# Performance work log

Measured on AMD Instinct MI355X. Metric: run time of the kernel, lower is better.

The kernel has to match this reference:

```python
import jax, jax.numpy as jnp
import numpy as np

D_MODEL = 1024
N_HEADS = 16
D_K = 64  # per-head dim and the scaling denominator used by the module
NEG = -1e9  # stand-in for -inf in masked_fill (rows are never fully masked)


def setup_inputs() -> dict:
    key = jax.random.key(0)
    ks = jax.random.split(key, 8)
    B, M, N = 2, 2048, 2048
    q = jax.random.normal(ks[0], (B, M, D_MODEL), dtype=jnp.float32)
    k = jax.random.normal(ks[1], (B, N, D_MODEL), dtype=jnp.float32)
    v = jax.random.normal(ks[2], (B, N, D_MODEL), dtype=jnp.float32)
    mask = jax.random.randint(ks[3], (B, M, N), 0, 2).astype(jnp.bool_)
    # xavier_uniform for square [d,d] weights: limit = sqrt(6/(d+d))
    lim = float(np.sqrt(6.0 / (D_MODEL + D_MODEL)))
    Wq = jax.random.uniform(ks[4], (D_MODEL, D_MODEL), jnp.float32, -lim, lim)
    Wk = jax.random.uniform(ks[5], (D_MODEL, D_MODEL), jnp.float32, -lim, lim)
    Wv = jax.random.uniform(ks[6], (D_MODEL, D_MODEL), jnp.float32, -lim, lim)
    Wo = jax.random.uniform(ks[7], (D_MODEL, D_MODEL), jnp.float32, -lim, lim)
    return {"q": q, "k": k, "v": v, "mask": mask,
            "Wq": Wq, "Wk": Wk, "Wv": Wv, "Wo": Wo}


def _split_heads(x):
    # (B, S, D) -> (B, H, S, Dh); the torch split/cat-on-batch trick is
    # mathematically identical to this standard head reshape.
    B, S, _ = x.shape
    return x.reshape(B, S, N_HEADS, D_K).transpose(0, 2, 1, 3)


def reference(q, k, v, mask, Wq, Wk, Wv, Wo):
    qw = _split_heads(q @ Wq.T)  # (B,H,M,Dh)
    kw = _split_heads(k @ Wk.T)  # (B,H,N,Dh)
    vw = _split_heads(v @ Wv.T)  # (B,H,N,Dh)
    scores = jnp.einsum('bhmd,bhnd->bhmn', qw, kw)
    scores = jnp.where(mask[:, None, :, :], NEG, scores)
    attn = jax.nn.softmax(scores / jnp.sqrt(jnp.float32(D_K)), axis=-1)
    ctx = jnp.einsum('bhmn,bhnd->bhmd', attn, vw)
    B, _, M, _ = ctx.shape
    ctx = ctx.transpose(0, 2, 1, 3).reshape(B, M, D_MODEL)
    return ctx @ Wo.T
```

## Files before the change

kernel.cpp:

```cpp
#include <hip/hip_runtime.h>
#include <hip/hip_bf16.h>
#include <stdint.h>
#include <string.h>

#define SEQ   2048
#define DM    1024
#define NH    16
#define NB    2

typedef __attribute__((ext_vector_type(8))) short bf16x8;
typedef __attribute__((ext_vector_type(4))) float f32x4;
typedef unsigned short u16;
typedef unsigned int   u32;

__device__ __forceinline__ u16 f2bf(float f) {
    u32 u = __float_as_uint(f);
    u += 0x7FFF + ((u >> 16) & 1);
    return (u16)(u >> 16);
}
__device__ __forceinline__ u32 pk2bf(float a, float b) {
    __hip_bfloat162 p = __float22bfloat162_rn(make_float2(a, b));
    u32 u; memcpy(&u, &p, 4); return u;
}
__device__ __forceinline__ float fexp2(float x) {
#if __has_builtin(__builtin_amdgcn_exp2f)
    return __builtin_amdgcn_exp2f(x);
#else
    return exp2f(x);
#endif
}
__device__ __forceinline__ float mask_exp2(float s, u32 lsel, int pos) {
#if __has_builtin(__builtin_amdgcn_sbfe)
    u32 keep = (u32)__builtin_amdgcn_sbfe((int)lsel, pos, 1);
#else
    u32 keep = (u32)((int)(lsel << (31 - pos)) >> 31);
#endif
    return __uint_as_float(__float_as_uint(fexp2(s)) & keep);
}
__device__ __forceinline__ void gl_lds16(const void* g, void* l) {
    __builtin_amdgcn_global_load_lds(
        (const __attribute__((address_space(1))) u32*)g,
        (__attribute__((address_space(3))) u32*)l, 16, 0, 0);
}
__device__ __forceinline__ void wbar_vm3() { asm volatile("s_waitcnt vmcnt(3)\ns_barrier" ::: "memory"); }
__device__ __forceinline__ void wbar_vm4() { asm volatile("s_waitcnt vmcnt(4)\ns_barrier" ::: "memory"); }
__device__ __forceinline__ void vm_drain() { asm volatile("s_waitcnt vmcnt(0)" ::: "memory"); }

struct CvtArgs {
    const float* s[7];
    u16* d[7];
    float scale[7];
    int start[8];
    const int* mask;
    u32* mbits;
};
__global__ __launch_bounds__(256) void cvt_kernel(CvtArgs a) {
    int bid = blockIdx.x;
    int tid = threadIdx.x;
    if (bid >= 8192) {
        int widx = (bid - 8192) * 256 + tid;
        uint4 v = ((const uint4*)a.mask)[widx];
        unsigned long long b0 = __ballot(v.x != 0);
        unsigned long long b1 = __ballot(v.y != 0);
        unsigned long long b2 = __ballot(v.z != 0);
        unsigned long long b3 = __ballot(v.w != 0);
        int lane = tid & 63;
        if (lane < 4) {
            int sh = lane * 16;
            u32 lo = (u32)((b0 >> sh) & 0xFFFF) | ((u32)((b1 >> sh) & 0xFFFF) << 16);
            u32 hi = (u32)((b2 >> sh) & 0xFFFF) | ((u32)((b3 >> sh) & 0xFFFF) << 16);
            size_t N = (size_t)(bid - 8192) * 1024 + (size_t)(tid >> 6) * 256
                     + (size_t)lane * 64;
            u32* dst = a.mbits + ((N >> 11) * 64 + ((N >> 6) & 31) * 2);
            *(uint2*)dst = make_uint2(lo, hi);
        }
        return;
    }
    int seg = 0;
#pragma unroll
    for (int i = 1; i < 7; ++i) if (bid >= a.start[i]) seg = i;
    float sc = a.scale[seg];
    size_t base = (size_t)(bid - a.start[seg]) * 2048 + tid * 8;
    const float4* s4 = (const float4*)(a.s[seg] + base);
    float4 x = s4[0], y = s4[1];
    u32 r[4];
    r[0] = pk2bf(x.x*sc, x.y*sc); r[1] = pk2bf(x.z*sc, x.w*sc);
    r[2] = pk2bf(y.x*sc, y.y*sc); r[3] = pk2bf(y.z*sc, y.w*sc);
    *(uint4*)(a.d[seg] + base) = *(uint4*)r;
}

template<int RT>
__device__ __forceinline__ void gemm_body(const u16* __restrict__ A,
                                          const u16* __restrict__ Bm,
                                          void* __restrict__ Y,
                                          int rtile, int ctile, int mode,
                                          u16* sA, u16* sB) {
    constexpr int ABUF = RT * 32 * 32;
    constexpr int BBUF = 128 * 32;
    const int tid  = threadIdx.x;
    const int wv   = tid >> 6, lane = tid & 63;
    const int quad = lane >> 4, ln = lane & 15;
    const int wr   = wv >> 1,  wc  = wv & 1;

    const int lr4 = lane >> 2;
    const int lcc = ((lane & 3) ^ ((lane >> 3) & 3)) * 8;

    const u16* gA[RT/2]; u16* lA[RT/2];
#pragma unroll
    for (int s = 0; s < RT/2; ++s) {
        int seg = wv * (RT/2) + s;
        gA[s] = A + (size_t)(rtile * (RT*32) + seg*16 + lr4) * 1024 + lcc;
        lA[s] = sA + seg * 512;
    }
    const u16* gB[2]; u16* lB[2];
#pragma unroll
    for (int s = 0; s < 2; ++s) {
        int seg = wv * 2 + s;
        gB[s] = Bm + (size_t)(ctile * 128 + seg*16 + lr4) * 1024 + lcc;
        lB[s] = sB + seg * 512;
    }

    f32x4 acc[RT][4];
#pragma unroll
    for (int i = 0; i < RT; ++i)
#pragma unroll
        for (int j = 0; j < 4; ++j) acc[i][j] = (f32x4){0.f,0.f,0.f,0.f};

    const int c0 = (quad ^ ((ln >> 1) & 3)) * 8;

#pragma unroll
    for (int s = 0; s < RT/2; ++s) gl_lds16(gA[s], lA[s]);
#pragma unroll
    for (int s = 0; s < 2; ++s)    gl_lds16(gB[s], lB[s]);
#pragma unroll
    for (int s = 0; s < RT/2; ++s) gl_lds16(gA[s] + 32, lA[s] + ABUF);
#pragma unroll
    for (int s = 0; s < 2; ++s)    gl_lds16(gB[s] + 32, lB[s] + BBUF);

    int bc = 0, bp = 2;
    for (int kt = 0; kt < 32; ++kt) {
        if (RT == 4) wbar_vm4(); else wbar_vm3();
        int pk = (kt + 2) & 31;
#pragma unroll
        for (int s = 0; s < RT/2; ++s) gl_lds16(gA[s] + pk*32, lA[s] + bp*ABUF);
#pragma unroll
        for (int s = 0; s < 2; ++s)    gl_lds16(gB[s] + pk*32, lB[s] + bp*BBUF);

        const u16* sAb = sA + bc * ABUF;
        const u16* sBb = sB + bc * BBUF;
        bf16x8 af[RT], bfr[4];
#pragma unroll
        for (int rt = 0; rt < RT; ++rt)
            af[rt] = *(const bf16x8*)(sAb + (wr*(RT*16) + rt*16 + ln) * 32 + c0);
#pragma unroll
        for (int ct = 0; ct < 4; ++ct)
            bfr[ct] = *(const bf16x8*)(sBb + (wc*64 + ct*16 + ln) * 32 + c0);
#pragma unroll
        for (int rt = 0; rt < RT; ++rt)
#pragma unroll
            for (int ct = 0; ct < 4; ++ct)
                acc[rt][ct] = __builtin_amdgcn_mfma_f32_16x16x32_bf16(
                    af[rt], bfr[ct], acc[rt][ct], 0, 0, 0);

        bc = (bc == 2) ? 0 : bc + 1;
        bp = (bp == 2) ? 0 : bp + 1;
    }
    vm_drain();

#pragma unroll
    for (int rt = 0; rt < RT; ++rt) {
#pragma unroll
        for (int ct = 0; ct < 4; ++ct) {
#pragma unroll
            for (int i = 0; i < 4; ++i) {
                int R = rtile*(RT*32) + wr*(RT*16) + rt*16 + quad*4 + i;
                int C = ctile*128 + wc*64 + ct*16 + ln;
                float val = acc[rt][ct][i];
                if (mode == 0) {
                    int b = R >> 11, s = R & 2047, h = C >> 6, d = C & 63;
                    ((u16*)Y)[((size_t)((b*NH + h) * SEQ + s) << 6) + d] = f2bf(val);
                } else if (mode == 1) {
                    int h = R >> 6, d = R & 63, b = C >> 11, n = C & 2047;
                    int nl = n & 63;
                    int np = (nl & 32) | (((nl & 15) >> 2) << 3) | (nl & 3)
                           | ((nl & 16) >> 2);
                    n = (n & ~63) | np;
                    ((u16*)Y)[((size_t)((b*NH + h) * 64 + d) << 11) + n] = f2bf(val);
                } else {
                    ((float*)Y)[(size_t)R * 1024 + C] = val;
                }
            }
        }
    }
}

struct QKVArgs { const u16* A[3]; const u16* B[3]; u16* Y[3]; };

__global__ __launch_bounds__(256) void gemm_qkv(QKVArgs g) {
    __shared__ u16 sA[3 * 128 * 32];
    __shared__ u16 sB[3 * 128 * 32];
    int z = blockIdx.z;
    if (z == 2)
        gemm_body<4>(g.A[2], g.B[2], g.Y[2], blockIdx.y, blockIdx.x, 1, sA, sB);
    else
        gemm_body<4>(g.A[z], g.B[z], g.Y[z], blockIdx.x, blockIdx.y, 0, sA, sB);
}

__global__ __launch_bounds__(256) void gemm_out(const u16* __restrict__ A,
                                                const u16* __restrict__ Bm,
                                                float* __restrict__ Y) {
    __shared__ u16 sA[3 * 64 * 32];
    __shared__ u16 sB[3 * 128 * 32];
    gemm_body<2>(A, Bm, Y, blockIdx.x, blockIdx.y, 2, sA, sB);
}

__global__ __launch_bounds__(512, 4) void attn_kernel(
    const u16* __restrict__ qw,
    const u16* __restrict__ kw,
    const u16* __restrict__ vt,
    const u32* __restrict__ mbits,
    u16* __restrict__ ctx) {

    __shared__ __align__(16) u16 smem[32768];
    u16* sK = smem;
    u16* sV = smem + 16384;

    const int mtile = blockIdx.x;
    const int bh    = blockIdx.y;
    const int b     = bh >> 4;
    const int tid   = threadIdx.x;
    const int wv    = tid >> 6, lane = tid & 63;
    const int quad  = lane >> 4, ln = lane & 15;
    const int m0    = mtile * 128;

    const size_t hbase = (size_t)bh * SEQ * 64;

    bf16x8 qf[2];
    {
        const u16* qp = qw + hbase + (size_t)(m0 + wv*16 + ln) * 64 + quad*8;
        qf[0] = *(const bf16x8*)(qp);
        qf[1] = *(const bf16x8*)(qp + 32);
    }

    f32x4 o[4], lsum;
    lsum = (f32x4){0.f,0.f,0.f,0.f};
#pragma unroll
    for (int j = 0; j < 4; ++j) o[j] = (f32x4){0.f,0.f,0.f,0.f};

    bf16x8 ones;
#pragma unroll
    for (int i = 0; i < 8; ++i) ones[i] = (short)0x3F80;

    const u32* mrow = mbits + (size_t)(b*SEQ + m0 + wv*16 + ln) * 64;

    const int lr = lane >> 3;
    const int lc = (lane & 7) ^ lr;
    const u16* gK = kw + hbase + (size_t)(wv*8 + lr) * 64 + lc*8;
    const u16* gV = vt + hbase + (size_t)(wv*8 + lr) * SEQ + lc*8;
    u16* lK = sK + wv * 512;
    u16* lV = sV + wv * 512;

    const int c0 = (quad ^ (ln & 7)) * 8;
    const u16* a1 = smem + ln*64 + c0;
    const u16* a2 = smem + ln*64 + (c0 ^ 32);

    gl_lds16(gK, lK);
    gl_lds16(gV, lV);
    uint2 wwA = *(const uint2*)(mrow);
    gl_lds16(gK + 4096, lK + 4096);
    gl_lds16(gV + 64,   lV + 4096);
    uint2 wwB = *(const uint2*)(mrow + 2);

    for (int mi = 0; mi < 8; ++mi) {
#pragma unroll
        for (int u = 0; u < 4; ++u) {
            const int bc = u;
            const int wb = (u + 2) & 3;
            wbar_vm3();
            int pidx = (mi*4 + u + 2) & 31;
            gl_lds16(gK + (size_t)pidx * 4096, lK + wb*4096);
            gl_lds16(gV + pidx * 64,           lV + wb*4096);
            uint2 wwC = *(const uint2*)(mrow + pidx*2);

            f32x4 s4[4];
            __builtin_amdgcn_s_setprio(1);
#pragma unroll
            for (int ct = 0; ct < 4; ++ct) {
                bf16x8 k0 = *(const bf16x8*)(a1 + bc*4096 + ct*1024);
                bf16x8 k1 = *(const bf16x8*)(a2 + bc*4096 + ct*1024);
                f32x4 z = (f32x4){0.f, 0.f, 0.f, 0.f};
                z = __builtin_amdgcn_mfma_f32_16x16x32_bf16(k0, qf[0], z, 0, 0, 0);
                z = __builtin_amdgcn_mfma_f32_16x16x32_bf16(k1, qf[1], z, 0, 0, 0);
                s4[ct] = z;
            }
            __builtin_amdgcn_s_setprio(0);

            u32 P0[4], P1[4];
            {
                u32 l0 = ~(wwA.x >> quad);
                u32 l1 = ~(wwA.y >> quad);
#pragma unroll
                for (int ct = 0; ct < 4; ++ct) {
                    float p[4];
                    p[0] = mask_exp2(s4[ct][0], l0, ct*4);
                    p[1] = mask_exp2(s4[ct][1], l0, 16 + ct*4);
                    p[2] = mask_exp2(s4[ct][2], l1, ct*4);
                    p[3] = mask_exp2(s4[ct][3], l1, 16 + ct*4);
                    u32 lo = pk2bf(p[0], p[1]);
                    u32 hi = pk2bf(p[2], p[3]);
                    if (ct == 0)      { P0[0] = lo; P0[1] = hi; }
                    else if (ct == 1) { P0[2] = lo; P0[3] = hi; }
                    else if (ct == 2) { P1[0] = lo; P1[1] = hi; }
                    else              { P1[2] = lo; P1[3] = hi; }
                }
            }
            bf16x8 pf0, pf1;
            memcpy(&pf0, P0, 16);
            memcpy(&pf1, P1, 16);

            __builtin_amdgcn_s_setprio(1);
            lsum = __builtin_amdgcn_mfma_f32_16x16x32_bf16(pf0, ones, lsum, 0, 0, 0);
            lsum = __builtin_amdgcn_mfma_f32_16x16x32_bf16(pf1, ones, lsum, 0, 0, 0);
#pragma unroll
            for (int ct = 0; ct < 4; ++ct) {
                bf16x8 vf0 = *(const bf16x8*)(a1 + 16384 + bc*4096 + ct*1024);
                bf16x8 vf1 = *(const bf16x8*)(a2 + 16384 + bc*4096 + ct*1024);
                o[ct] = __builtin_amdgcn_mfma_f32_16x16x32_bf16(pf0, vf0, o[ct], 0, 0, 0);
                o[ct] = __builtin_amdgcn_mfma_f32_16x16x32_bf16(pf1, vf1, o[ct], 0, 0, 0);
            }
            __builtin_amdgcn_s_setprio(0);

            wwA = wwB; wwB = wwC;
        }
    }
    vm_drain();

#pragma unroll
    for (int i = 0; i < 4; ++i) {
        float inv = 1.f / lsum[i];
        int m = m0 + wv*16 + quad*4 + i;
        size_t base = ((size_t)(b * SEQ + m) << 10) + (bh & 15) * 64;
#pragma unroll
        for (int ct = 0; ct < 4; ++ct)
            ctx[base + ct*16 + ln] = f2bf(o[ct][i] * inv);
    }
}

extern "C" void kernel_launch(void* const* d_in, const int* in_sizes, int n_in,
                              void* d_out, int out_size, void* d_ws, size_t ws_size,
                              hipStream_t stream) {
    const float* q    = (const float*)d_in[0];
    const float* k    = (const float*)d_in[1];
    const float* v    = (const float*)d_in[2];
    const int*   mask = (const int*)d_in[3];
    const float* Wq   = (const float*)d_in[4];
    const float* Wk   = (const float*)d_in[5];
    const float* Wv   = (const float*)d_in[6];
    const float* Wo   = (const float*)d_in[7];
    float* out = (float*)d_out;

    char* ws = (char*)d_ws;
    const size_t SZH = (size_t)NB * SEQ * DM * 2;
    const size_t SZW = (size_t)DM * DM * 2;
    u16* qw   = (u16*)(ws);
    u16* kw   = (u16*)(ws + SZH);
    u16* vt   = (u16*)(ws + 2*SZH);
    u16* ctx  = (u16*)(ws + 3*SZH);
    u16* vb   = ctx;
    u32* mbits= (u32*)(ws + 4*SZH);
    u16* qb   = (u16*)(ws + 4*SZH + (1u<<20));
    u16* kb   = (u16*)(ws + 4*SZH + (1u<<20) + SZH);
    u16* Wqb  = (u16*)(ws + 4*SZH + (1u<<20) + 2*SZH);
    u16* Wkb  = (u16*)((char*)Wqb + SZW);
    u16* Wvb  = (u16*)((char*)Wqb + 2*SZW);
    u16* Wob  = (u16*)((char*)Wqb + 3*SZW);

    const float CSC = 0.18033688011112042f;

    CvtArgs ca;
    ca.s[0]=q;  ca.d[0]=qb;  ca.scale[0]=1.f;
    ca.s[1]=k;  ca.d[1]=kb;  ca.scale[1]=1.f;
    ca.s[2]=v;  ca.d[2]=vb;  ca.scale[2]=1.f;
    ca.s[3]=Wq; ca.d[3]=Wqb; ca.scale[3]=CSC;
    ca.s[4]=Wk; ca.d[4]=Wkb; ca.scale[4]=1.f;
    ca.s[5]=Wv; ca.d[5]=Wvb; ca.scale[5]=1.f;
    ca.s[6]=Wo; ca.d[6]=Wob; ca.scale[6]=1.f;
    int st[8] = {0, 2048, 4096, 6144, 6656, 7168, 7680, 8192};
    for (int i = 0; i < 8; ++i) ca.start[i] = st[i];
    ca.mask  = mask;
    ca.mbits = mbits;
    cvt_kernel<<<dim3(16384), dim3(256), 0, stream>>>(ca);

    QKVArgs ga;
    ga.A[0]=qb;  ga.B[0]=Wqb; ga.Y[0]=qw;
    ga.A[1]=kb;  ga.B[1]=Wkb; ga.Y[1]=kw;
    ga.A[2]=Wvb; ga.B[2]=vb;  ga.Y[2]=vt;
    gemm_qkv<<<dim3(32, 8, 3), dim3(256), 0, stream>>>(ga);

    attn_kernel<<<dim3(SEQ/128, NB*NH), dim3(512), 0, stream>>>(qw, kw, vt, mbits, ctx);

    gemm_out<<<dim3(64, 8), dim3(256), 0, stream>>>(ctx, Wob, out);
}
```

Measured before the change: 242.8 us.

## Fuse conversion and QKV projection into one cooperative kernel with grid sync

Merges the fp32-to-bf16 conversion/mask-bitpacking kernel and the QKV projection GEMM into one cooperative kernel of 768 persistent blocks. The conversion work is grid-strided, then a grid-wide sync separates it from the GEMM tiles, which are remapped so neighbouring blocks share tiles. This removes one kernel launch and its ramp-down/ramp-up gap. It adds a grid barrier cost and lowers parallelism in the conversion phase, and it falls back to the two separate launches if the cooperative launch fails.

Result: slower. 358.4 us (+47.6%).

```diff
diff --git a/kernel.cpp b/kernel.cpp
--- a/kernel.cpp
+++ b/kernel.cpp
@@ -1,7 +1,10 @@
 #include <hip/hip_runtime.h>
 #include <hip/hip_bf16.h>
+#include <hip/hip_cooperative_groups.h>
 #include <stdint.h>
 #include <string.h>
+
+namespace cg = cooperative_groups;
 
 #define SEQ   2048
 #define DM    1024
@@ -54,11 +57,10 @@
     const int* mask;
     u32* mbits;
 };
-__global__ __launch_bounds__(256) void cvt_kernel(CvtArgs a) {
-    int bid = blockIdx.x;
+__device__ __forceinline__ void cvt_work(const CvtArgs& a, int vb) {
     int tid = threadIdx.x;
-    if (bid >= 8192) {
-        int widx = (bid - 8192) * 256 + tid;
+    if (vb >= 8192) {
+        int widx = (vb - 8192) * 256 + tid;
         uint4 v = ((const uint4*)a.mask)[widx];
         unsigned long long b0 = __ballot(v.x != 0);
         unsigned long long b1 = __ballot(v.y != 0);
@@ -69,7 +71,7 @@
             int sh = lane * 16;
             u32 lo = (u32)((b0 >> sh) & 0xFFFF) | ((u32)((b1 >> sh) & 0xFFFF) << 16);
             u32 hi = (u32)((b2 >> sh) & 0xFFFF) | ((u32)((b3 >> sh) & 0xFFFF) << 16);
-            size_t N = (size_t)(bid - 8192) * 1024 + (size_t)(tid >> 6) * 256
+            size_t N = (size_t)(vb - 8192) * 1024 + (size_t)(tid >> 6) * 256
                      + (size_t)lane * 64;
             u32* dst = a.mbits + ((N >> 11) * 64 + ((N >> 6) & 31) * 2);
             *(uint2*)dst = make_uint2(lo, hi);
@@ -78,15 +80,19 @@
     }
     int seg = 0;
 #pragma unroll
-    for (int i = 1; i < 7; ++i) if (bid >= a.start[i]) seg = i;
+    for (int i = 1; i < 7; ++i) if (vb >= a.start[i]) seg = i;
     float sc = a.scale[seg];
-    size_t base = (size_t)(bid - a.start[seg]) * 2048 + tid * 8;
+    size_t base = (size_t)(vb - a.start[seg]) * 2048 + tid * 8;
     const float4* s4 = (const float4*)(a.s[seg] + base);
     float4 x = s4[0], y = s4[1];
     u32 r[4];
     r[0] = pk2bf(x.x*sc, x.y*sc); r[1] = pk2bf(x.z*sc, x.w*sc);
     r[2] = pk2bf(y.x*sc, y.y*sc); r[3] = pk2bf(y.z*sc, y.w*sc);
     *(uint4*)(a.d[seg] + base) = *(uint4*)r;
+}
+
+__global__ __launch_bounds__(256) void cvt_kernel(CvtArgs a) {
+    cvt_work(a, blockIdx.x);
 }
 
 template<int RT>
@@ -206,6 +212,23 @@
         gemm_body<4>(g.A[z], g.B[z], g.Y[z], blockIdx.x, blockIdx.y, 0, sA, sB);
 }
 
+__global__ __launch_bounds__(256, 3) void fused_pre(CvtArgs ca, QKVArgs ga) {
+    for (int it = 0; it < 22; ++it) {
+        int vb = it * 768 + (int)blockIdx.x;
+        if (vb < 16384) cvt_work(ca, vb);
+    }
+    cg::this_grid().sync();
+    __shared__ u16 sA[3 * 128 * 32];
+    __shared__ u16 sB[3 * 128 * 32];
+    int x = (int)blockIdx.x & 7, j = (int)blockIdx.x >> 3;
+    int t = x * 96 + j;
+    int z = t >> 8, rem = t & 255;
+    if (z == 2)
+        gemm_body<4>(ga.A[2], ga.B[2], ga.Y[2], rem & 7, rem >> 3, 1, sA, sB);
+    else
+        gemm_body<4>(ga.A[z], ga.B[z], ga.Y[z], rem >> 3, rem & 7, 0, sA, sB);
+}
+
 __global__ __launch_bounds__(256) void gemm_out(const u16* __restrict__ A,
                                                 const u16* __restrict__ Bm,
                                                 float* __restrict__ Y) {
@@ -389,13 +412,21 @@
     for (int i = 0; i < 8; ++i) ca.start[i] = st[i];
     ca.mask  = mask;
     ca.mbits = mbits;
-    cvt_kernel<<<dim3(16384), dim3(256), 0, stream>>>(ca);
 
     QKVArgs ga;
     ga.A[0]=qb;  ga.B[0]=Wqb; ga.Y[0]=qw;
     ga.A[1]=kb;  ga.B[1]=Wkb; ga.Y[1]=kw;
     ga.A[2]=Wvb; ga.B[2]=vb;  ga.Y[2]=vt;
-    gemm_qkv<<<dim3(32, 8, 3), dim3(256), 0, stream>>>(ga);
+
+    void* kargs[] = { (void*)&ca, (void*)&ga };
+    hipError_t ce = hipLaunchCooperativeKernel((const void*)fused_pre,
+                                               dim3(768), dim3(256),
+                                               kargs, 0, stream);
+    if (ce != hipSuccess) {
+        (void)hipGetLastError();
+        cvt_kernel<<<dim3(16384), dim3(256), 0, stream>>>(ca);
+        gemm_qkv<<<dim3(32, 8, 3), dim3(256), 0, stream>>>(ga);
+    }
 
     attn_kernel<<<dim3(SEQ/128, NB*NH), dim3(512), 0, stream>>>(qw, kw, vt, mbits, ctx);
 
```

## Split key columns across two wave groups so each K/V fragment serves two query tiles

Applied to the files above, without the earlier changes.

The attention kernel's eight waves are regrouped into two groups of four. Each wave now owns 32 query rows (two 16-row tiles) and handles half of each key block, so every K and V fragment read from LDS feeds two MFMA tiles instead of one. The two groups' partial outputs and row sums are combined through LDS at the end before normalisation and the bf16 store. This cuts LDS read traffic per MFMA. In exchange it adds register pressure, an extra mask-word load per step, and a shared-memory reduction with two extra barriers in the epilogue.

Result: slower. 251.2 us, median of 2 (+3.5%).

```diff
diff --git a/kernel.cpp b/kernel.cpp
--- a/kernel.cpp
+++ b/kernel.cpp
@@ -231,27 +231,34 @@
     const int tid   = threadIdx.x;
     const int wv    = tid >> 6, lane = tid & 63;
     const int quad  = lane >> 4, ln = lane & 15;
+    const int g     = wv >> 2;
+    const int w2    = wv & 3;
     const int m0    = mtile * 128;
 
     const size_t hbase = (size_t)bh * SEQ * 64;
 
-    bf16x8 qf[2];
-    {
-        const u16* qp = qw + hbase + (size_t)(m0 + wv*16 + ln) * 64 + quad*8;
-        qf[0] = *(const bf16x8*)(qp);
-        qf[1] = *(const bf16x8*)(qp + 32);
-    }
-
-    f32x4 o[4], lsum;
-    lsum = (f32x4){0.f,0.f,0.f,0.f};
-#pragma unroll
-    for (int j = 0; j < 4; ++j) o[j] = (f32x4){0.f,0.f,0.f,0.f};
+    bf16x8 qf[2][2];
+#pragma unroll
+    for (int mt = 0; mt < 2; ++mt) {
+        const u16* qp = qw + hbase + (size_t)(m0 + w2*32 + mt*16 + ln) * 64 + quad*8;
+        qf[mt][0] = *(const bf16x8*)(qp);
+        qf[mt][1] = *(const bf16x8*)(qp + 32);
+    }
+
+    f32x4 o[2][4], lsum[2];
+#pragma unroll
+    for (int mt = 0; mt < 2; ++mt) {
+        lsum[mt] = (f32x4){0.f,0.f,0.f,0.f};
+#pragma unroll
+        for (int j = 0; j < 4; ++j) o[mt][j] = (f32x4){0.f,0.f,0.f,0.f};
+    }
 
     bf16x8 ones;
 #pragma unroll
     for (int i = 0; i < 8; ++i) ones[i] = (short)0x3F80;
 
-    const u32* mrow = mbits + (size_t)(b*SEQ + m0 + wv*16 + ln) * 64;
+    const u32* mrow0 = mbits + (size_t)(b*SEQ + m0 + w2*32 + ln) * 64;
+    const u32* mrow1 = mrow0 + ((size_t)16 * 64);
 
     const int lr = lane >> 3;
     const int lc = (lane & 7) ^ lr;
@@ -263,86 +270,116 @@
     const int c0 = (quad ^ (ln & 7)) * 8;
     const u16* a1 = smem + ln*64 + c0;
     const u16* a2 = smem + ln*64 + (c0 ^ 32);
+    const u16* aK1 = a1 + g*2048;
+    const u16* aK2 = a2 + g*2048;
+    const u16* aV  = (g ? a2 : a1) + 16384;
+    const int  msh = g*8 + quad;
 
     gl_lds16(gK, lK);
     gl_lds16(gV, lV);
-    uint2 wwA = *(const uint2*)(mrow);
+    uint2 wA0 = *(const uint2*)(mrow0);
+    uint2 wA1 = *(const uint2*)(mrow1);
     gl_lds16(gK + 4096, lK + 4096);
     gl_lds16(gV + 64,   lV + 4096);
-    uint2 wwB = *(const uint2*)(mrow + 2);
+    uint2 wB0 = *(const uint2*)(mrow0 + 2);
+    uint2 wB1 = *(const uint2*)(mrow1 + 2);
 
     for (int mi = 0; mi < 8; ++mi) {
 #pragma unroll
         for (int u = 0; u < 4; ++u) {
             const int bc = u;
             const int wb = (u + 2) & 3;
-            wbar_vm3();
+            wbar_vm4();
             int pidx = (mi*4 + u + 2) & 31;
             gl_lds16(gK + (size_t)pidx * 4096, lK + wb*4096);
             gl_lds16(gV + pidx * 64,           lV + wb*4096);
-            uint2 wwC = *(const uint2*)(mrow + pidx*2);
-
-            f32x4 s4[4];
+            uint2 wC0 = *(const uint2*)(mrow0 + pidx*2);
+            uint2 wC1 = *(const uint2*)(mrow1 + pidx*2);
+
+            f32x4 s4[2][2];
             __builtin_amdgcn_s_setprio(1);
 #pragma unroll
+            for (int ct2 = 0; ct2 < 2; ++ct2) {
+                bf16x8 k0 = *(const bf16x8*)(aK1 + bc*4096 + ct2*1024);
+                bf16x8 k1 = *(const bf16x8*)(aK2 + bc*4096 + ct2*1024);
+#pragma unroll
+                for (int mt = 0; mt < 2; ++mt) {
+                    f32x4 z = (f32x4){0.f, 0.f, 0.f, 0.f};
+                    z = __builtin_amdgcn_mfma_f32_16x16x32_bf16(k0, qf[mt][0], z, 0, 0, 0);
+                    z = __builtin_amdgcn_mfma_f32_16x16x32_bf16(k1, qf[mt][1], z, 0, 0, 0);
+                    s4[mt][ct2] = z;
+                }
+            }
+            __builtin_amdgcn_s_setprio(0);
+
+            bf16x8 pfm[2];
+#pragma unroll
+            for (int mt = 0; mt < 2; ++mt) {
+                u32 wx = mt ? wA1.x : wA0.x;
+                u32 wy = mt ? wA1.y : wA0.y;
+                u32 l0 = ~(wx >> msh);
+                u32 l1 = ~(wy >> msh);
+                u32 P[4];
+#pragma unroll
+                for (int ct2 = 0; ct2 < 2; ++ct2) {
+                    float p[4];
+                    p[0] = mask_exp2(s4[mt][ct2][0], l0, ct2*4);
+                    p[1] = mask_exp2(s4[mt][ct2][1], l0, 16 + ct2*4);
+                    p[2] = mask_exp2(s4[mt][ct2][2], l1, ct2*4);
+                    p[3] = mask_exp2(s4[mt][ct2][3], l1, 16 + ct2*4);
+                    P[ct2*2]     = pk2bf(p[0], p[1]);
+                    P[ct2*2 + 1] = pk2bf(p[2], p[3]);
+                }
+                memcpy(&pfm[mt], P, 16);
+            }
+
+            __builtin_amdgcn_s_setprio(1);
+            lsum[0] = __builtin_amdgcn_mfma_f32_16x16x32_bf16(pfm[0], ones, lsum[0], 0, 0, 0);
+            lsum[1] = __builtin_amdgcn_mfma_f32_16x16x32_bf16(pfm[1], ones, lsum[1], 0, 0, 0);
+#pragma unroll
             for (int ct = 0; ct < 4; ++ct) {
-                bf16x8 k0 = *(const bf16x8*)(a1 + bc*4096 + ct*1024);
-                bf16x8 k1 = *(const bf16x8*)(a2 + bc*4096 + ct*1024);
-                f32x4 z = (f32x4){0.f, 0.f, 0.f, 0.f};
-                z = __builtin_amdgcn_mfma_f32_16x16x32_bf16(k0, qf[0], z, 0, 0, 0);
-                z = __builtin_amdgcn_mfma_f32_16x16x32_bf16(k1, qf[1], z, 0, 0, 0);
-                s4[ct] = z;
+                bf16x8 vf = *(const bf16x8*)(aV + bc*4096 + ct*1024);
+                o[0][ct] = __builtin_amdgcn_mfma_f32_16x16x32_bf16(pfm[0], vf, o[0][ct], 0, 0, 0);
+                o[1][ct] = __builtin_amdgcn_mfma_f32_16x16x32_bf16(pfm[1], vf, o[1][ct], 0, 0, 0);
             }
             __builtin_amdgcn_s_setprio(0);
 
-            u32 P0[4], P1[4];
-            {
-                u32 l0 = ~(wwA.x >> quad);
-                u32 l1 = ~(wwA.y >> quad);
-#pragma unroll
-                for (int ct = 0; ct < 4; ++ct) {
-                    float p[4];
-                    p[0] = mask_exp2(s4[ct][0], l0, ct*4);
-                    p[1] = mask_exp2(s4[ct][1], l0, 16 + ct*4);
-                    p[2] = mask_exp2(s4[ct][2], l1, ct*4);
-                    p[3] = mask_exp2(s4[ct][3], l1, 16 + ct*4);
-                    u32 lo = pk2bf(p[0], p[1]);
-                    u32 hi = pk2bf(p[2], p[3]);
-                    if (ct == 0)      { P0[0] = lo; P0[1] = hi; }
-                    else if (ct == 1) { P0[2] = lo; P0[3] = hi; }
-                    else if (ct == 2) { P1[0] = lo; P1[1] = hi; }
-                    else              { P1[2] = lo; P1[3] = hi; }
-                }
-            }
-            bf16x8 pf0, pf1;
-            memcpy(&pf0, P0, 16);
-            memcpy(&pf1, P1, 16);
-
-            __builtin_amdgcn_s_setprio(1);
-            lsum = __builtin_amdgcn_mfma_f32_16x16x32_bf16(pf0, ones, lsum, 0, 0, 0);
-            lsum = __builtin_amdgcn_mfma_f32_16x16x32_bf16(pf1, ones, lsum, 0, 0, 0);
-#pragma unroll
-            for (int ct = 0; ct < 4; ++ct) {
-                bf16x8 vf0 = *(const bf16x8*)(a1 + 16384 + bc*4096 + ct*1024);
-                bf16x8 vf1 = *(const bf16x8*)(a2 + 16384 + bc*4096 + ct*1024);
-                o[ct] = __builtin_amdgcn_mfma_f32_16x16x32_bf16(pf0, vf0, o[ct], 0, 0, 0);
-                o[ct] = __builtin_amdgcn_mfma_f32_16x16x32_bf16(pf1, vf1, o[ct], 0, 0, 0);
-            }
-            __builtin_amdgcn_s_setprio(0);
-
-            wwA = wwB; wwB = wwC;
+            wA0 = wB0; wA1 = wB1;
+            wB0 = wC0; wB1 = wC1;
         }
     }
     vm_drain();
-
-#pragma unroll
-    for (int i = 0; i < 4; ++i) {
-        float inv = 1.f / lsum[i];
-        int m = m0 + wv*16 + quad*4 + i;
-        size_t base = ((size_t)(b * SEQ + m) << 10) + (bh & 15) * 64;
-#pragma unroll
-        for (int ct = 0; ct < 4; ++ct)
-            ctx[base + ct*16 + ln] = f2bf(o[ct][i] * inv);
+    __syncthreads();
+
+    float* sO  = (float*)smem;
+    float* sLs = (float*)((char*)smem + 34816);
+    if (g == 1) {
+#pragma unroll
+        for (int mt = 0; mt < 2; ++mt)
+#pragma unroll
+            for (int i = 0; i < 4; ++i) {
+                int lm = w2*32 + mt*16 + quad*4 + i;
+                sLs[lm] = lsum[mt][i];
+#pragma unroll
+                for (int ct = 0; ct < 4; ++ct)
+                    sO[lm*68 + ct*16 + ln] = o[mt][ct][i];
+            }
+    }
+    __syncthreads();
+    if (g == 0) {
+#pragma unroll
+        for (int mt = 0; mt < 2; ++mt)
+#pragma unroll
+            for (int i = 0; i < 4; ++i) {
+                int lm = w2*32 + mt*16 + quad*4 + i;
+                float inv = 1.f / (lsum[mt][i] + sLs[lm]);
+                int m = m0 + lm;
+                size_t base = ((size_t)(b * SEQ + m) << 10) + (bh & 15) * 64;
+#pragma unroll
+                for (int ct = 0; ct < 4; ++ct)
+                    ctx[base + ct*16 + ln] =
+                        f2bf((o[mt][ct][i] + sO[lm*68 + ct*16 + ln]) * inv);
+            }
     }
 }
 
```
